# Optimization experiments

Hardware: AMD Instinct MI355X
Metric: run time of the kernel (lower is better)

Reference implementation:

```python
import jax, jax.numpy as jnp
import numpy as np

N_NODES = 50000
N_EDGES = 800000
D_FEAT = 128
HIDDEN = 256
N_CLASSES = 2


def setup_inputs() -> dict:
    key = jax.random.key(0)
    ks = jax.random.split(key, 9)
    x = jax.random.normal(ks[0], (N_NODES, D_FEAT), dtype=jnp.float32)
    edge_index = jax.random.randint(ks[1], (2, N_EDGES), 0, N_NODES, dtype=jnp.int32)
    # SAGEConv params: lin_l (applied to aggregated neighbors), lin_r (root), bias
    s1 = 1.0 / np.sqrt(D_FEAT)
    s2 = 1.0 / np.sqrt(HIDDEN)
    W1l = jax.random.normal(ks[2], (D_FEAT, HIDDEN), dtype=jnp.float32) * s1
    W1r = jax.random.normal(ks[3], (D_FEAT, HIDDEN), dtype=jnp.float32) * s1
    b1 = jax.random.normal(ks[4], (HIDDEN,), dtype=jnp.float32) * s1
    W2l = jax.random.normal(ks[5], (HIDDEN, N_CLASSES), dtype=jnp.float32) * s2
    W2r = jax.random.normal(ks[6], (HIDDEN, N_CLASSES), dtype=jnp.float32) * s2
    b2 = jax.random.normal(ks[7], (N_CLASSES,), dtype=jnp.float32) * s2
    return {"x": x, "edge_index": edge_index, "W1l": W1l, "W1r": W1r,
            "b1": b1, "W2l": W2l, "W2r": W2r, "b2": b2}


def _sage_conv(x, src, dst, Wl, Wr, b):
    # mean-aggregate neighbor features x[src] into destination nodes
    n = x.shape[0]
    agg = jax.ops.segment_sum(x[src], dst, num_segments=n)  # [N, d]
    deg = jax.ops.segment_sum(jnp.ones((src.shape[0],), x.dtype), dst,
                              num_segments=n)
    mean = agg / jnp.maximum(deg, 1.0)[:, None]
    return mean @ Wl + x @ Wr + b


def reference(x, edge_index, W1l, W1r, b1, W2l, W2r, b2):
    src, dst = edge_index[0], edge_index[1]
    h = jax.nn.relu(_sage_conv(x, src, dst, W1l, W1r, b1))
    embeddings = h  # dropout is identity in eval mode
    out = jax.nn.sigmoid(_sage_conv(embeddings, src, dst, W2l, W2r, b2))
    return out, embeddings
```

## Files before the change

### kernel.cpp

```cpp
#include <hip/hip_runtime.h>
#include <math.h>

#define N_NODES 50000
#define N_EDGES 800000
#define D_FEAT 128
#define HIDDEN 256
#define NB_SCAN 196
#define GEMM_BLOCKS 782

#define AGG_B 2048

#define NSLICE 32
#define SLICE_E 25000
#define NPART 2
#define PART_N 25000
#define NTASK 64

#define CVT_B 512
#define PH_B (NTASK + CVT_B)
#define SCAT_B 3125

typedef __bf16 bf16x8 __attribute__((ext_vector_type(8)));
typedef float f32x4 __attribute__((ext_vector_type(4)));

__device__ __forceinline__ unsigned f2b(float f) {
    unsigned u = __builtin_bit_cast(unsigned, f);
    return (u + 0x7fff + ((u >> 16) & 1)) >> 16;
}

__global__ __launch_bounds__(256) void prep_hist(
    const float* __restrict__ x, const int* __restrict__ dst,
    const float* __restrict__ W1l, const float* __restrict__ W1r,
    unsigned* __restrict__ arr, unsigned short* __restrict__ rank,
    unsigned* __restrict__ xb, unsigned short* __restrict__ Wfrag) {
    __shared__ unsigned hist[PART_N / 2 + 8];
    int b = blockIdx.x;
    int t = threadIdx.x;
    if (b < NTASK) {
        int slice = b >> 1, part = b & 1;
        int lo = part * PART_N;
        for (int k = t; k < PART_N / 2; k += 256) hist[k] = 0;
        __syncthreads();
        int e0 = slice * SLICE_E;
        for (int k = t; k < SLICE_E; k += 256) {
            int e = e0 + k;
            int d = dst[e];
            unsigned dl = (unsigned)(d - lo);
            if (dl < (unsigned)PART_N) {
                unsigned old = atomicAdd(&hist[dl >> 1], (dl & 1) ? 65536u : 1u);
                rank[e] = (unsigned short)((old >> ((dl & 1) << 4)) & 0xffffu);
            }
        }
        __syncthreads();
        for (int k = t; k < PART_N; k += 256)
            arr[(size_t)slice * N_NODES + lo + k] =
                (hist[k >> 1] >> ((k & 1) << 4)) & 0xffffu;
    } else {
        int cb = b - NTASK;
        for (int g = cb * 256 + t; g < 800000; g += CVT_B * 256) {
            float4 v0 = *(const float4*)(x + (size_t)g * 8);
            float4 v1 = *(const float4*)(x + (size_t)g * 8 + 4);
            uint4 o;
            o.x = f2b(v0.x) | (f2b(v0.y) << 16);
            o.y = f2b(v0.z) | (f2b(v0.w) << 16);
            o.z = f2b(v1.x) | (f2b(v1.y) << 16);
            o.w = f2b(v1.z) | (f2b(v1.w) << 16);
            int d = g >> 4;
            int j = (g & 15) << 2;
            *(uint4*)(xb + (size_t)d * 64 + j) = o;
        }
        for (int tt = cb * 256 + t; tt < 65536; tt += CVT_B * 256) {
            int j = tt & 7;
            int lane = (tt >> 3) & 63;
            int ks = (tt >> 9) & 7;
            int nt = tt >> 12;
            int k = ks * 32 + ((lane >> 4) << 3) + j;
            int n = (nt << 4) + (lane & 15);
            float v = (k < 128) ? W1l[k * 256 + n] : W1r[(k - 128) * 256 + n];
            Wfrag[tt] = (unsigned short)f2b(v);
        }
    }
}

__global__ void scan1(const unsigned* __restrict__ arr, int* __restrict__ cnt,
                      int* __restrict__ bsum) {
    __shared__ int tmp[256];
    int t = threadIdx.x;
    int i = blockIdx.x * 256 + t;
    int c = 0;
    if (i < N_NODES) {
#pragma unroll 8
        for (int k = 0; k < NSLICE; k++) c += (int)arr[(size_t)k * N_NODES + i];
        cnt[i] = c;
    }
    tmp[t] = c;
    __syncthreads();
    for (int off = 128; off > 0; off >>= 1) {
        if (t < off) tmp[t] += tmp[t + off];
        __syncthreads();
    }
    if (t == 0) bsum[blockIdx.x] = tmp[0];
}

__global__ void scanB(const int* __restrict__ cnt, const int* __restrict__ bsum,
                      int* __restrict__ rowbeg, unsigned* __restrict__ arr) {
    __shared__ int bs[256];
    __shared__ int tmp[256];
    int t = threadIdx.x;
    int b = blockIdx.x;
    bs[t] = (t < NB_SCAN) ? bsum[t] : 0;
    __syncthreads();
    for (int off = 1; off < 256; off <<= 1) {
        int y = (t >= off) ? bs[t - off] : 0;
        __syncthreads();
        bs[t] += y;
        __syncthreads();
    }
    int boff = (b == 0) ? 0 : bs[b - 1];
    int i = b * 256 + t;
    int v = (i < N_NODES) ? cnt[i] : 0;
    tmp[t] = v;
    __syncthreads();
    for (int off = 1; off < 256; off <<= 1) {
        int y = (t >= off) ? tmp[t - off] : 0;
        __syncthreads();
        tmp[t] += y;
        __syncthreads();
    }
    if (i < N_NODES) {
        unsigned running = (unsigned)(tmp[t] - v + boff);
        rowbeg[i] = (int)running;
#pragma unroll 8
        for (int k = 0; k < NSLICE; k++) {
            unsigned old = arr[(size_t)k * N_NODES + i];
            arr[(size_t)k * N_NODES + i] = running;
            running += old;
        }
    }
}

__global__ __launch_bounds__(256) void scatter2(
    const int* __restrict__ src, const int* __restrict__ dst,
    const unsigned* __restrict__ arr, const unsigned short* __restrict__ rank,
    unsigned short* __restrict__ esrc) {
    int e = blockIdx.x * 256 + threadIdx.x;
    if (e < N_EDGES) {
        int slice = e / SLICE_E;
        int d = dst[e];
        unsigned pos = arr[(size_t)slice * N_NODES + d] + (unsigned)rank[e];
        esrc[pos] = (unsigned short)src[e];
    }
}

__global__ __launch_bounds__(256) void agg1(
    const unsigned* __restrict__ xb, unsigned* __restrict__ mb,
    const unsigned short* __restrict__ esrc,
    const int* __restrict__ rowbeg, const int* __restrict__ cnt) {
    int wid = (blockIdx.x * 256 + threadIdx.x) >> 6;
    int lane = threadIdx.x & 63;
    int g = lane >> 4;
    int i = lane & 15;
    for (int d = wid; d < N_NODES; d += AGG_B * 4) {
        int beg = rowbeg[d];
        int c = cnt[d];
        int end = beg + c;
        float acc[8];
#pragma unroll
        for (int f = 0; f < 8; f++) acc[f] = 0.0f;

        for (int base = beg; base < end; base += 64) {
            int m = end - base; if (m > 64) m = 64;
            int idx = base + lane;
            int e = (int)esrc[idx < end ? idx : end - 1];
            for (int j0 = 0; j0 < m; j0 += 4) {
                int ss = __shfl(e, j0 + g);
                float sc = (j0 + g < m) ? 1.0f : 0.0f;
                uint4 u = *(const uint4*)(xb + (size_t)ss * 64 + (i << 2));
                acc[0] += sc * __builtin_bit_cast(float, u.x << 16);
                acc[1] += sc * __builtin_bit_cast(float, u.x & 0xffff0000u);
                acc[2] += sc * __builtin_bit_cast(float, u.y << 16);
                acc[3] += sc * __builtin_bit_cast(float, u.y & 0xffff0000u);
                acc[4] += sc * __builtin_bit_cast(float, u.z << 16);
                acc[5] += sc * __builtin_bit_cast(float, u.z & 0xffff0000u);
                acc[6] += sc * __builtin_bit_cast(float, u.w << 16);
                acc[7] += sc * __builtin_bit_cast(float, u.w & 0xffff0000u);
            }
        }
#pragma unroll
        for (int f = 0; f < 8; f++) {
            acc[f] += __shfl_xor(acc[f], 16);
            acc[f] += __shfl_xor(acc[f], 32);
        }
        if (lane < 16) {
            float inv = 1.0f / fmaxf((float)c, 1.0f);
            uint4 o;
            o.x = f2b(acc[0] * inv) | (f2b(acc[1] * inv) << 16);
            o.y = f2b(acc[2] * inv) | (f2b(acc[3] * inv) << 16);
            o.z = f2b(acc[4] * inv) | (f2b(acc[5] * inv) << 16);
            o.w = f2b(acc[6] * inv) | (f2b(acc[7] * inv) << 16);
            *(uint4*)(mb + (size_t)d * 64 + (i << 2)) = o;
        }
    }
}

__global__ __launch_bounds__(256) void gemm1ps(
    const unsigned* __restrict__ mb, const unsigned* __restrict__ xb,
    const unsigned short* __restrict__ Wfrag, const float* __restrict__ b1,
    const float* __restrict__ W2l, const float* __restrict__ W2r,
    const float* __restrict__ b2,
    float* __restrict__ h, float* __restrict__ p, float* __restrict__ s) {
    __shared__ unsigned A[64 * 128];
    __shared__ float ppart[64][4];

    int r0 = blockIdx.x * 64;
    int tid = threadIdx.x;
    int w = tid >> 6;
    int lane = tid & 63;
    int quad = lane >> 4;
    int l15 = lane & 15;

    ((float*)ppart)[tid] = 0.0f;

    int sr = tid >> 3;
    int c0 = tid & 7;
#pragma unroll
    for (int jj = 0; jj < 2; jj++) {
        int row = (jj << 5) + sr;
#pragma unroll
        for (int j = 0; j < 4; j++) {
            int c = c0 + (j << 3);
            uint4 v;
            if (c < 16) v = *(const uint4*)(mb + (size_t)(r0 + row) * 64 + (c << 2));
            else        v = *(const uint4*)(xb + (size_t)(r0 + row) * 64 + ((c - 16) << 2));
            int cp = c ^ (row & 7);
            *(uint4*)(A + row * 128 + (cp << 2)) = v;
        }
    }
    __syncthreads();

    f32x4 acc[16];
#pragma unroll
    for (int i = 0; i < 16; i++) acc[i] = (f32x4){0.0f, 0.0f, 0.0f, 0.0f};

    for (int ks = 0; ks < 8; ks++) {
        bf16x8 bfr[4];
#pragma unroll
        for (int nt = 0; nt < 4; nt++) {
            int ntg = (w << 2) + nt;
            uint4 raw = *(const uint4*)(Wfrag + ((((ntg << 3) + ks) << 6) + lane) * 8);
            bfr[nt] = __builtin_bit_cast(bf16x8, raw);
        }
#pragma unroll
        for (int mt = 0; mt < 4; mt++) {
            int row = (mt << 4) + l15;
            int c = (ks << 2) + quad;
            uint4 araw = *(const uint4*)(A + row * 128 + ((c ^ (row & 7)) << 2));
            bf16x8 afr = __builtin_bit_cast(bf16x8, araw);
#pragma unroll
            for (int nt = 0; nt < 4; nt++) {
                acc[(mt << 2) + nt] = __builtin_amdgcn_mfma_f32_16x16x32_bf16(
                    afr, bfr[nt], acc[(mt << 2) + nt], 0, 0, 0);
            }
        }
    }

    float w2[4][4];
#pragma unroll
    for (int nt = 0; nt < 4; nt++) {
        int col = (w << 6) + (nt << 4) + l15;
        float2 l2 = *(const float2*)(W2l + col * 2);
        float2 r2 = *(const float2*)(W2r + col * 2);
        w2[nt][0] = l2.x; w2[nt][1] = l2.y; w2[nt][2] = r2.x; w2[nt][3] = r2.y;
    }

#pragma unroll
    for (int mt = 0; mt < 4; mt++) {
        float red[4][4];
#pragma unroll
        for (int v = 0; v < 4; v++)
#pragma unroll
            for (int r = 0; r < 4; r++) red[v][r] = 0.0f;

#pragma unroll
        for (int nt = 0; nt < 4; nt++) {
            int col = (w << 6) + (nt << 4) + l15;
            float b = b1[col];
            f32x4 v = acc[(mt << 2) + nt];
#pragma unroll
            for (int r = 0; r < 4; r++) {
                float hv = v[r] + b;
                hv = hv > 0.0f ? hv : 0.0f;
                int row = r0 + (mt << 4) + (quad << 2) + r;
                if (row < N_NODES)
                    __builtin_nontemporal_store(hv, &h[(size_t)row * 256 + col]);
                red[0][r] += hv * w2[nt][0];
                red[1][r] += hv * w2[nt][1];
                red[2][r] += hv * w2[nt][2];
                red[3][r] += hv * w2[nt][3];
            }
        }
#pragma unroll
        for (int v = 0; v < 4; v++)
#pragma unroll
            for (int r = 0; r < 4; r++) {
                red[v][r] += __shfl_xor(red[v][r], 1);
                red[v][r] += __shfl_xor(red[v][r], 2);
                red[v][r] += __shfl_xor(red[v][r], 4);
                red[v][r] += __shfl_xor(red[v][r], 8);
            }
        if (l15 == 0) {
            int lrow = (mt << 4) + (quad << 2);
#pragma unroll
            for (int r = 0; r < 4; r++)
#pragma unroll
                for (int v = 0; v < 4; v++)
                    atomicAdd(&ppart[lrow + r][v], red[v][r]);
        }
    }
    __syncthreads();

    if (tid < 64) {
        int row = r0 + tid;
        if (row < N_NODES) {
            float2 pv = {ppart[tid][0], ppart[tid][1]};
            float2 sv = {ppart[tid][2] + b2[0], ppart[tid][3] + b2[1]};
            *(float2*)(p + (size_t)row * 2) = pv;
            *(float2*)(s + (size_t)row * 2) = sv;
        }
    }
}

__global__ __launch_bounds__(256) void agg2(
    const float* __restrict__ p, const float* __restrict__ s,
    const unsigned short* __restrict__ esrc,
    const int* __restrict__ rowbeg, const int* __restrict__ cnt,
    float* __restrict__ out) {
    int wid = (blockIdx.x * 256 + threadIdx.x) >> 6;
    int lane = threadIdx.x & 63;
    for (int d = wid; d < N_NODES; d += AGG_B * 4) {
        int beg = rowbeg[d];
        int c = cnt[d];
        int end = beg + c;
        float a0 = 0.0f, a1 = 0.0f;
        for (int base = beg; base < end; base += 64) {
            int idx = base + lane;
            if (idx < end) {
                int ss = (int)esrc[idx];
                float2 v = *(const float2*)(p + (size_t)ss * 2);
                a0 += v.x; a1 += v.y;
            }
        }
#pragma unroll
        for (int off = 32; off > 0; off >>= 1) {
            a0 += __shfl_down(a0, off);
            a1 += __shfl_down(a1, off);
        }
        if (lane == 0) {
            float inv = 1.0f / fmaxf((float)c, 1.0f);
            float z0 = a0 * inv + s[(size_t)d * 2 + 0];
            float z1 = a1 * inv + s[(size_t)d * 2 + 1];
            float2 o = {1.0f / (1.0f + expf(-z0)), 1.0f / (1.0f + expf(-z1))};
            *(float2*)(out + (size_t)d * 2) = o;
        }
    }
}

extern "C" void kernel_launch(void* const* d_in, const int* in_sizes, int n_in,
                              void* d_out, int out_size, void* d_ws, size_t ws_size,
                              hipStream_t stream) {
    const float* x   = (const float*)d_in[0];
    const int*   ei  = (const int*)d_in[1];
    const float* W1l = (const float*)d_in[2];
    const float* W1r = (const float*)d_in[3];
    const float* b1  = (const float*)d_in[4];
    const float* W2l = (const float*)d_in[5];
    const float* W2r = (const float*)d_in[6];
    const float* b2  = (const float*)d_in[7];

    const int* src = ei;
    const int* dst = ei + N_EDGES;

    float* out = (float*)d_out;
    float* emb = out + (size_t)N_NODES * 2;

    int* cnt    = (int*)d_ws;
    int* rowbeg = cnt + N_NODES;
    int* bsum   = rowbeg + N_NODES;
    unsigned short* esrc = (unsigned short*)(bsum + 256);
    unsigned* xb = (unsigned*)(esrc + 800064);
    unsigned* mb = xb + (size_t)50048 * 64;
    unsigned* arr = mb;
    unsigned short* Wfrag = (unsigned short*)(mb + (size_t)50048 * 64);
    float* p = (float*)(Wfrag + 65536);
    float* s = p + (size_t)N_NODES * 2;
    unsigned short* rank = (unsigned short*)emb;

    prep_hist<<<PH_B, 256, 0, stream>>>(x, dst, W1l, W1r, arr, rank, xb, Wfrag);
    scan1<<<NB_SCAN, 256, 0, stream>>>(arr, cnt, bsum);
    scanB<<<NB_SCAN, 256, 0, stream>>>(cnt, bsum, rowbeg, arr);
    scatter2<<<SCAT_B, 256, 0, stream>>>(src, dst, arr, rank, esrc);

    agg1<<<AGG_B, 256, 0, stream>>>(xb, mb, esrc, rowbeg, cnt);

    gemm1ps<<<GEMM_BLOCKS, 256, 0, stream>>>(mb, xb, Wfrag, b1, W2l, W2r, b2,
                                             emb, p, s);

    agg2<<<AGG_B, 256, 0, stream>>>(p, s, esrc, rowbeg, cnt, out);
}
```

Baseline: 227.2 us.

## Replace sliced LDS histogram CSR build with global atomic counting

Drops the 32-slice by 2-partition shared-memory histogram that wrote per-slice counts to a large array and scanned them. Instead each edge does a global atomicAdd on its destination's count to get its rank, and the scan and scatter use just the count and row-begin arrays. This removes the 32x50000 slice array traffic, the per-slice prefix loops and the 64-block serial histogram phase. In exchange it adds a memset launch and relies on global atomics with random contention. Edge order within each row becomes nondeterministic.

Result: faster. 215.5 us (-5.1%).

```diff
diff --git a/kernel.cpp b/kernel.cpp
--- a/kernel.cpp
+++ b/kernel.cpp
@@ -10,14 +10,9 @@
 
 #define AGG_B 2048
 
-#define NSLICE 32
-#define SLICE_E 25000
-#define NPART 2
-#define PART_N 25000
-#define NTASK 64
-
 #define CVT_B 512
-#define PH_B (NTASK + CVT_B)
+#define CNT_B 3125
+#define CP_B (CVT_B + CNT_B)
 #define SCAT_B 3125
 
 typedef __bf16 bf16x8 __attribute__((ext_vector_type(8)));
@@ -28,36 +23,15 @@
     return (u + 0x7fff + ((u >> 16) & 1)) >> 16;
 }
 
-__global__ __launch_bounds__(256) void prep_hist(
+__global__ __launch_bounds__(256) void count_prep(
     const float* __restrict__ x, const int* __restrict__ dst,
     const float* __restrict__ W1l, const float* __restrict__ W1r,
-    unsigned* __restrict__ arr, unsigned short* __restrict__ rank,
+    int* __restrict__ cnt, unsigned short* __restrict__ rank,
     unsigned* __restrict__ xb, unsigned short* __restrict__ Wfrag) {
-    __shared__ unsigned hist[PART_N / 2 + 8];
     int b = blockIdx.x;
     int t = threadIdx.x;
-    if (b < NTASK) {
-        int slice = b >> 1, part = b & 1;
-        int lo = part * PART_N;
-        for (int k = t; k < PART_N / 2; k += 256) hist[k] = 0;
-        __syncthreads();
-        int e0 = slice * SLICE_E;
-        for (int k = t; k < SLICE_E; k += 256) {
-            int e = e0 + k;
-            int d = dst[e];
-            unsigned dl = (unsigned)(d - lo);
-            if (dl < (unsigned)PART_N) {
-                unsigned old = atomicAdd(&hist[dl >> 1], (dl & 1) ? 65536u : 1u);
-                rank[e] = (unsigned short)((old >> ((dl & 1) << 4)) & 0xffffu);
-            }
-        }
-        __syncthreads();
-        for (int k = t; k < PART_N; k += 256)
-            arr[(size_t)slice * N_NODES + lo + k] =
-                (hist[k >> 1] >> ((k & 1) << 4)) & 0xffffu;
-    } else {
-        int cb = b - NTASK;
-        for (int g = cb * 256 + t; g < 800000; g += CVT_B * 256) {
+    if (b < CVT_B) {
+        for (int g = b * 256 + t; g < 800000; g += CVT_B * 256) {
             float4 v0 = *(const float4*)(x + (size_t)g * 8);
             float4 v1 = *(const float4*)(x + (size_t)g * 8 + 4);
             uint4 o;
@@ -69,7 +43,7 @@
             int j = (g & 15) << 2;
             *(uint4*)(xb + (size_t)d * 64 + j) = o;
         }
-        for (int tt = cb * 256 + t; tt < 65536; tt += CVT_B * 256) {
+        for (int tt = b * 256 + t; tt < 65536; tt += CVT_B * 256) {
             int j = tt & 7;
             int lane = (tt >> 3) & 63;
             int ks = (tt >> 9) & 7;
@@ -79,20 +53,20 @@
             float v = (k < 128) ? W1l[k * 256 + n] : W1r[(k - 128) * 256 + n];
             Wfrag[tt] = (unsigned short)f2b(v);
         }
-    }
-}
-
-__global__ void scan1(const unsigned* __restrict__ arr, int* __restrict__ cnt,
-                      int* __restrict__ bsum) {
+    } else {
+        int e = (b - CVT_B) * 256 + t;
+        if (e < N_EDGES) {
+            int d = dst[e];
+            rank[e] = (unsigned short)atomicAdd(&cnt[d], 1);
+        }
+    }
+}
+
+__global__ void scan1(const int* __restrict__ cnt, int* __restrict__ bsum) {
     __shared__ int tmp[256];
     int t = threadIdx.x;
     int i = blockIdx.x * 256 + t;
-    int c = 0;
-    if (i < N_NODES) {
-#pragma unroll 8
-        for (int k = 0; k < NSLICE; k++) c += (int)arr[(size_t)k * N_NODES + i];
-        cnt[i] = c;
-    }
+    int c = (i < N_NODES) ? cnt[i] : 0;
     tmp[t] = c;
     __syncthreads();
     for (int off = 128; off > 0; off >>= 1) {
@@ -103,7 +77,7 @@
 }
 
 __global__ void scanB(const int* __restrict__ cnt, const int* __restrict__ bsum,
-                      int* __restrict__ rowbeg, unsigned* __restrict__ arr) {
+                      int* __restrict__ rowbeg) {
     __shared__ int bs[256];
     __shared__ int tmp[256];
     int t = threadIdx.x;
@@ -127,27 +101,17 @@
         tmp[t] += y;
         __syncthreads();
     }
-    if (i < N_NODES) {
-        unsigned running = (unsigned)(tmp[t] - v + boff);
-        rowbeg[i] = (int)running;
-#pragma unroll 8
-        for (int k = 0; k < NSLICE; k++) {
-            unsigned old = arr[(size_t)k * N_NODES + i];
-            arr[(size_t)k * N_NODES + i] = running;
-            running += old;
-        }
-    }
+    if (i < N_NODES) rowbeg[i] = tmp[t] - v + boff;
 }
 
 __global__ __launch_bounds__(256) void scatter2(
     const int* __restrict__ src, const int* __restrict__ dst,
-    const unsigned* __restrict__ arr, const unsigned short* __restrict__ rank,
+    const int* __restrict__ rowbeg, const unsigned short* __restrict__ rank,
     unsigned short* __restrict__ esrc) {
     int e = blockIdx.x * 256 + threadIdx.x;
     if (e < N_EDGES) {
-        int slice = e / SLICE_E;
         int d = dst[e];
-        unsigned pos = arr[(size_t)slice * N_NODES + d] + (unsigned)rank[e];
+        unsigned pos = (unsigned)rowbeg[d] + (unsigned)rank[e];
         esrc[pos] = (unsigned short)src[e];
     }
 }
@@ -389,16 +353,17 @@
     unsigned short* esrc = (unsigned short*)(bsum + 256);
     unsigned* xb = (unsigned*)(esrc + 800064);
     unsigned* mb = xb + (size_t)50048 * 64;
-    unsigned* arr = mb;
     unsigned short* Wfrag = (unsigned short*)(mb + (size_t)50048 * 64);
     float* p = (float*)(Wfrag + 65536);
     float* s = p + (size_t)N_NODES * 2;
     unsigned short* rank = (unsigned short*)emb;
 
-    prep_hist<<<PH_B, 256, 0, stream>>>(x, dst, W1l, W1r, arr, rank, xb, Wfrag);
-    scan1<<<NB_SCAN, 256, 0, stream>>>(arr, cnt, bsum);
-    scanB<<<NB_SCAN, 256, 0, stream>>>(cnt, bsum, rowbeg, arr);
-    scatter2<<<SCAT_B, 256, 0, stream>>>(src, dst, arr, rank, esrc);
+    hipMemsetAsync(cnt, 0, N_NODES * sizeof(int), stream);
+
+    count_prep<<<CP_B, 256, 0, stream>>>(x, dst, W1l, W1r, cnt, rank, xb, Wfrag);
+    scan1<<<NB_SCAN, 256, 0, stream>>>(cnt, bsum);
+    scanB<<<NB_SCAN, 256, 0, stream>>>(cnt, bsum, rowbeg);
+    scatter2<<<SCAT_B, 256, 0, stream>>>(src, dst, rowbeg, rank, esrc);
 
     agg1<<<AGG_B, 256, 0, stream>>>(xb, mb, esrc, rowbeg, cnt);
 
```
